# Kernel tuning notes

Measured on AMD Instinct MI355X. Metric: run time of the kernel, lower is better.

## Reference

```python
import jax, jax.numpy as jnp
import numpy as np

N, E, IN, HID, HEADS, ED, OUT = 50000, 600000, 128, 64, 4, 16, 2
NEG_SLOPE = 0.2  # PyG GATv2Conv default negative_slope


def glorot(key, shape):
    fan_in, fan_out = shape[0], shape[-1]
    s = jnp.sqrt(6.0 / (fan_in + fan_out))
    return jax.random.uniform(key, shape, jnp.float32, -s, s)


def setup_inputs() -> dict:
    key = jax.random.key(0)
    ks = jax.random.split(key, 16)
    return {
        "x": jax.random.normal(ks[0], (N, IN), jnp.float32),
        "edge_index": jax.random.randint(ks[1], (2, E), 0, N, jnp.int32),
        "edge_attr": jax.random.normal(ks[2], (E, ED), jnp.float32),
        # conv1: GATv2Conv(IN -> HID, heads=HEADS, concat=True, edge_dim=ED)
        "W1l": glorot(ks[3], (IN, HEADS * HID)), "b1l": jnp.zeros((HEADS * HID,), jnp.float32),
        "W1r": glorot(ks[4], (IN, HEADS * HID)), "b1r": jnp.zeros((HEADS * HID,), jnp.float32),
        "W1e": glorot(ks[5], (ED, HEADS * HID)), "b1e": jnp.zeros((HEADS * HID,), jnp.float32),
        "att1": glorot(ks[6], (HEADS, HID)),
        "bias1": jnp.zeros((HEADS * HID,), jnp.float32),
        # conv2: GATv2Conv(HEADS*HID -> HID, heads=1, concat=False, edge_dim=ED)
        "W2l": glorot(ks[7], (HEADS * HID, HID)), "b2l": jnp.zeros((HID,), jnp.float32),
        "W2r": glorot(ks[8], (HEADS * HID, HID)), "b2r": jnp.zeros((HID,), jnp.float32),
        "W2e": glorot(ks[9], (ED, HID)), "b2e": jnp.zeros((HID,), jnp.float32),
        "att2": glorot(ks[10], (1, HID)),
        "bias2": jnp.zeros((HID,), jnp.float32),
        # edge MLP: Linear(2*HID+ED -> HID) -> ReLU -> Linear(HID -> OUT)
        "Wm1": glorot(ks[11], (2 * HID + ED, HID)), "bm1": jnp.zeros((HID,), jnp.float32),
        "Wm2": glorot(ks[12], (HID, OUT)), "bm2": jnp.zeros((OUT,), jnp.float32),
    }


def gatv2_layer(x, src, dst, edge_attr, Wl, bl, Wr, br, We, be, att, bias, heads, ch, concat):
    n = x.shape[0]
    xl = (x @ Wl + bl).reshape(n, heads, ch)          # lin_l(source)
    xr = (x @ Wr + br).reshape(n, heads, ch)          # lin_r(target)
    xe = (edge_attr @ We + be).reshape(-1, heads, ch)  # lin_edge(edge_attr)
    m = jax.nn.leaky_relu(xl[src] + xr[dst] + xe, NEG_SLOPE)   # [E, H, C]
    logits = jnp.einsum('ehc,hc->eh', m, att)                  # [E, H]
    # segment softmax over incoming edges of each target node
    amax = jax.lax.stop_gradient(jax.ops.segment_max(logits, dst, num_segments=n))
    ex = jnp.exp(logits - amax[dst])
    denom = jax.ops.segment_sum(ex, dst, num_segments=n)
    alpha = ex / denom[dst]                                    # [E, H]
    out = jax.ops.segment_sum(xl[src] * alpha[..., None], dst, num_segments=n)  # [N, H, C]
    out = out.reshape(n, heads * ch) if concat else out.mean(axis=1)
    return out + bias


def reference(x, edge_index, edge_attr, W1l, b1l, W1r, b1r, W1e, b1e, att1, bias1,
              W2l, b2l, W2r, b2r, W2e, b2e, att2, bias2, Wm1, bm1, Wm2, bm2):
    src, dst = edge_index[0], edge_index[1]
    h = jax.nn.relu(gatv2_layer(x, src, dst, edge_attr, W1l, b1l, W1r, b1r, W1e, b1e, att1, bias1, HEADS, HID, True))
    h = jax.nn.relu(gatv2_layer(h, src, dst, edge_attr, W2l, b2l, W2r, b2r, W2e, b2e, att2, bias2, 1, HID, False))
    ef = jnp.concatenate([h[src], h[dst], edge_attr], axis=1)  # [E, 2*HID+ED]
    return jax.nn.relu(ef @ Wm1 + bm1) @ Wm2 + bm2             # [E, OUT]
```

## Files before the change

kernel.cpp:

```cpp
#include <hip/hip_runtime.h>
#include <math.h>

#define NN 50000
#define EE 600000
#define IND 128
#define HIDD 64
#define NH 4
#define EDD 16
#define OUTD 2
#define C1 256

typedef _Float16 h2 __attribute__((ext_vector_type(2)));

__device__ __forceinline__ float lrelu(float v){ return v > 0.f ? v : 0.2f*v; }
__device__ __forceinline__ unsigned short f2bf(float f){
    unsigned b = __float_as_uint(f);
    b += 0x7FFF + ((b >> 16) & 1);
    return (unsigned short)(b >> 16);
}
__device__ __forceinline__ float bf2f(unsigned short h){
    return __uint_as_float(((unsigned)h) << 16);
}

#if defined(__has_builtin)
#if __has_builtin(__builtin_amdgcn_fdot2)
#define HAS_FDOT2 1
#endif
#endif
__device__ __forceinline__ float fdot2(h2 a, h2 b, float c){
#ifdef HAS_FDOT2
    return __builtin_amdgcn_fdot2(a, b, c, false);
#else
    return fmaf((float)a[1], (float)b[1], fmaf((float)a[0], (float)b[0], c));
#endif
}

__global__ __launch_bounds__(256) void k_hist(const int* __restrict__ dst, int* __restrict__ cnt)
{
    int stride = gridDim.x * blockDim.x;
    for (int e = blockIdx.x * blockDim.x + threadIdx.x; e < EE; e += stride)
        atomicAdd(&cnt[dst[e]], 1);
}

__global__ __launch_bounds__(1024) void k_scan(const int* __restrict__ cnt, int* __restrict__ rs)
{
    __shared__ int wsum[16];
    __shared__ int wpref[16];
    int t = threadIdx.x, lane = t & 63, w = t >> 6;
    int running = 0;
    for (int base = 0; base < NN; base += 1024) {
        int idx = base + t;
        int v = (idx < NN) ? cnt[idx] : 0;
        int sc = v;
#pragma unroll
        for (int off = 1; off < 64; off <<= 1) {
            int u = __shfl_up(sc, off, 64);
            if (lane >= off) sc += u;
        }
        if (lane == 63) wsum[w] = sc;
        __syncthreads();
        if (w == 0 && lane < 16) {
            int x = wsum[lane];
#pragma unroll
            for (int off = 1; off < 16; off <<= 1) {
                int u = __shfl_up(x, off, 64);
                if (lane >= off) x += u;
            }
            wpref[lane] = x;
        }
        __syncthreads();
        int woff = (w == 0) ? 0 : wpref[w - 1];
        if (idx < NN) rs[idx] = running + woff + sc - v;
        running += wpref[15];
        __syncthreads();
    }
    if (t == 0) rs[NN] = running;
}

__global__ __launch_bounds__(256) void k_scatter(
    const int* __restrict__ src, const int* __restrict__ dst,
    const float* __restrict__ ea,
    const int* __restrict__ rs, int* __restrict__ cur,
    int* __restrict__ esrc, _Float16* __restrict__ ea_s, _Float16* __restrict__ ea_h)
{
    int stride = gridDim.x * blockDim.x;
    for (int e = blockIdx.x * blockDim.x + threadIdx.x; e < EE; e += stride) {
        int d = dst[e];
        int p = rs[d] + atomicAdd(&cur[d], 1);
        esrc[p] = src[e];
        const float4* s4 = (const float4*)(ea + (size_t)e * EDD);
        float4 a0 = s4[0], a1 = s4[1], a2 = s4[2], a3 = s4[3];
        union { h2 h[8]; uint4 u[2]; } pk;
        pk.h[0][0] = (_Float16)a0.x; pk.h[0][1] = (_Float16)a0.y;
        pk.h[1][0] = (_Float16)a0.z; pk.h[1][1] = (_Float16)a0.w;
        pk.h[2][0] = (_Float16)a1.x; pk.h[2][1] = (_Float16)a1.y;
        pk.h[3][0] = (_Float16)a1.z; pk.h[3][1] = (_Float16)a1.w;
        pk.h[4][0] = (_Float16)a2.x; pk.h[4][1] = (_Float16)a2.y;
        pk.h[5][0] = (_Float16)a2.z; pk.h[5][1] = (_Float16)a2.w;
        pk.h[6][0] = (_Float16)a3.x; pk.h[6][1] = (_Float16)a3.y;
        pk.h[7][0] = (_Float16)a3.z; pk.h[7][1] = (_Float16)a3.w;
        uint4* dq = (uint4*)(ea_s + (size_t)p * EDD);
        dq[0] = pk.u[0]; dq[1] = pk.u[1];
        uint4* hq = (uint4*)(ea_h + (size_t)e * EDD);
        hq[0] = pk.u[0]; hq[1] = pk.u[1];
    }
}

__global__ __launch_bounds__(256) void k_lin1(
    const float* __restrict__ x, const float* __restrict__ Wl, const float* __restrict__ bl,
    const float* __restrict__ Wr, const float* __restrict__ br,
    unsigned short* __restrict__ xl, float* __restrict__ xr)
{
    __shared__ float As[16 * IND];
    int t = threadIdx.x;
    int row0 = blockIdx.x * 16;
#pragma unroll
    for (int j = 0; j < 8; ++j) {
        int idx = t + j * 256;
        int r = idx >> 7, c = idx & 127;
        As[idx] = (row0 + r < NN) ? x[(size_t)(row0 + r) * IND + c] : 0.f;
    }
    __syncthreads();
    float accl[16], accr[16];
    float bL = bl[t], bR = br[t];
#pragma unroll
    for (int i = 0; i < 16; ++i) { accl[i] = bL; accr[i] = bR; }
    for (int k = 0; k < IND; k += 4) {
        float wl0 = Wl[(k+0) * C1 + t], wl1 = Wl[(k+1) * C1 + t];
        float wl2 = Wl[(k+2) * C1 + t], wl3 = Wl[(k+3) * C1 + t];
        float wr0 = Wr[(k+0) * C1 + t], wr1 = Wr[(k+1) * C1 + t];
        float wr2 = Wr[(k+2) * C1 + t], wr3 = Wr[(k+3) * C1 + t];
#pragma unroll
        for (int i = 0; i < 16; ++i) {
            float4 a = *((const float4*)&As[i * IND + k]);
            accl[i] = fmaf(a.x, wl0, accl[i]); accl[i] = fmaf(a.y, wl1, accl[i]);
            accl[i] = fmaf(a.z, wl2, accl[i]); accl[i] = fmaf(a.w, wl3, accl[i]);
            accr[i] = fmaf(a.x, wr0, accr[i]); accr[i] = fmaf(a.y, wr1, accr[i]);
            accr[i] = fmaf(a.z, wr2, accr[i]); accr[i] = fmaf(a.w, wr3, accr[i]);
        }
    }
#pragma unroll
    for (int i = 0; i < 16; ++i) {
        int r = row0 + i;
        if (r < NN) {
            xl[(size_t)r * C1 + t] = f2bf(accl[i]);
            xr[(size_t)r * C1 + t] = accr[i];
        }
    }
}

#define GAT1_EDGE(XU, U0, U1) {                                                \
    float4 xl4 = make_float4(bf2f((XU).x), bf2f((XU).y), bf2f((XU).z), bf2f((XU).w)); \
    union { uint4 u[2]; h2 h[8]; } eu_; eu_.u[0] = (U0); eu_.u[1] = (U1);      \
    float xex = sb4.x, xey = sb4.y, xez = sb4.z, xew = sb4.w;                  \
    _Pragma("unroll")                                                          \
    for (int kk = 0; kk < 8; ++kk) {                                           \
        h2 ev2 = eu_.h[kk];                                                    \
        xex = fdot2(ev2, Wh[0][kk], xex);                                      \
        xey = fdot2(ev2, Wh[1][kk], xey);                                      \
        xez = fdot2(ev2, Wh[2][kk], xez);                                      \
        xew = fdot2(ev2, Wh[3][kk], xew);                                      \
    }                                                                          \
    float vx = lrelu(xl4.x + xr4.x + xex);                                     \
    float vy = lrelu(xl4.y + xr4.y + xey);                                     \
    float vz = lrelu(xl4.z + xr4.z + xez);                                     \
    float vw = lrelu(xl4.w + xr4.w + xew);                                     \
    float p = vx * sa4.x + vy * sa4.y + vz * sa4.z + vw * sa4.w;               \
    p += __shfl_xor(p, 1, 64);                                                 \
    p += __shfl_xor(p, 2, 64);                                                 \
    p += __shfl_xor(p, 4, 64);                                                 \
    p += __shfl_xor(p, 8, 64);                                                 \
    float mn = fmaxf(m, p);                                                    \
    float scl = __expf(m - mn);                                                \
    float el  = __expf(p - mn);                                                \
    den = fmaf(den, scl, el);                                                  \
    acc.x = fmaf(acc.x, scl, el * xl4.x);                                      \
    acc.y = fmaf(acc.y, scl, el * xl4.y);                                      \
    acc.z = fmaf(acc.z, scl, el * xl4.z);                                      \
    acc.w = fmaf(acc.w, scl, el * xl4.w);                                      \
    m = mn;                                                                    \
}

__global__ __launch_bounds__(256, 3) void k_gat1(
    const int* __restrict__ rs, const int* __restrict__ esrc,
    const _Float16* __restrict__ ea_s, const float* __restrict__ We, const float* __restrict__ be,
    const float* __restrict__ att, const unsigned short* __restrict__ xl,
    const float* __restrict__ xr, float* __restrict__ h1)
{
    int t = threadIdx.x, lane = t & 63, w = t >> 6;
    int c4 = lane * 4;
    h2 Wh[4][8];
#pragma unroll
    for (int k = 0; k < 16; ++k) {
        float4 wv = *((const float4*)(We + k * C1 + c4));
        Wh[0][k>>1][k&1] = (_Float16)wv.x;
        Wh[1][k>>1][k&1] = (_Float16)wv.y;
        Wh[2][k>>1][k&1] = (_Float16)wv.z;
        Wh[3][k>>1][k&1] = (_Float16)wv.w;
    }
    float4 sb4 = *((const float4*)(be + c4));
    float4 sa4 = *((const float4*)(att + c4));
    for (int n = blockIdx.x * 4 + w; n < NN; n += gridDim.x * 4) {
        int beg = __builtin_amdgcn_readfirstlane(rs[n]);
        int end = __builtin_amdgcn_readfirstlane(rs[n + 1]);
        float4 xr4 = *((const float4*)(xr + (size_t)n * C1 + c4));
        float m = -INFINITY, den = 0.f;
        float4 acc = make_float4(0.f, 0.f, 0.f, 0.f);
        int i = beg;
        for (; i + 2 <= end; i += 2) {
            int s0 = esrc[i], s1 = esrc[i + 1];
            ushort4 xu0 = *((const ushort4*)(xl + (size_t)s0 * C1 + c4));
            ushort4 xu1 = *((const ushort4*)(xl + (size_t)s1 * C1 + c4));
            const uint4* ep = (const uint4*)(ea_s + (size_t)i * EDD);
            uint4 u00 = ep[0], u01 = ep[1];
            uint4 u10 = ep[2], u11 = ep[3];
            GAT1_EDGE(xu0, u00, u01);
            GAT1_EDGE(xu1, u10, u11);
        }
        if (i < end) {
            int s0 = esrc[i];
            ushort4 xu0 = *((const ushort4*)(xl + (size_t)s0 * C1 + c4));
            const uint4* ep = (const uint4*)(ea_s + (size_t)i * EDD);
            uint4 u00 = ep[0], u01 = ep[1];
            GAT1_EDGE(xu0, u00, u01);
        }
        float r = den > 0.f ? 1.f / den : 0.f;
        float4 o = make_float4(acc.x * r, acc.y * r, acc.z * r, acc.w * r);
        *((float4*)(h1 + (size_t)n * C1 + c4)) = o;
    }
}

__global__ __launch_bounds__(256) void k_lin2(
    const float* __restrict__ h1acc, const float* __restrict__ bias1,
    const float* __restrict__ Wl, const float* __restrict__ bl,
    const float* __restrict__ Wr, const float* __restrict__ br,
    unsigned short* __restrict__ xl2, float* __restrict__ xr2)
{
    __shared__ float As[16 * 260];
    int t = threadIdx.x;
    int row0 = blockIdx.x * 16;
    float b1 = bias1[t];
#pragma unroll
    for (int j = 0; j < 16; ++j) {
        float v = (row0 + j < NN) ? h1acc[(size_t)(row0 + j) * C1 + t] : 0.f;
        v = v + b1;
        As[j * 260 + t] = v > 0.f ? v : 0.f;
    }
    __syncthreads();
    int col = t & 63, g = t >> 6;
    float accl[4], accr[4];
    float bL = bl[col], bR = br[col];
#pragma unroll
    for (int i = 0; i < 4; ++i) { accl[i] = bL; accr[i] = bR; }
    for (int k = 0; k < C1; k += 4) {
        float wl0 = Wl[(k+0) * HIDD + col], wl1 = Wl[(k+1) * HIDD + col];
        float wl2 = Wl[(k+2) * HIDD + col], wl3 = Wl[(k+3) * HIDD + col];
        float wr0 = Wr[(k+0) * HIDD + col], wr1 = Wr[(k+1) * HIDD + col];
        float wr2 = Wr[(k+2) * HIDD + col], wr3 = Wr[(k+3) * HIDD + col];
#pragma unroll
        for (int i = 0; i < 4; ++i) {
            float4 a = *((const float4*)&As[(g * 4 + i) * 260 + k]);
            accl[i] = fmaf(a.x, wl0, accl[i]); accl[i] = fmaf(a.y, wl1, accl[i]);
            accl[i] = fmaf(a.z, wl2, accl[i]); accl[i] = fmaf(a.w, wl3, accl[i]);
            accr[i] = fmaf(a.x, wr0, accr[i]); accr[i] = fmaf(a.y, wr1, accr[i]);
            accr[i] = fmaf(a.z, wr2, accr[i]); accr[i] = fmaf(a.w, wr3, accr[i]);
        }
    }
#pragma unroll
    for (int i = 0; i < 4; ++i) {
        int r = row0 + g * 4 + i;
        if (r < NN) {
            xl2[(size_t)r * HIDD + col] = f2bf(accl[i]);
            xr2[(size_t)r * HIDD + col] = accr[i];
        }
    }
}

#define GAT2_EDGE(XU, U0, U1) {                                                \
    float xlv = bf2f(XU);                                                      \
    union { uint4 u[2]; h2 h[8]; } eu_; eu_.u[0] = (U0); eu_.u[1] = (U1);      \
    float xe = bev;                                                            \
    _Pragma("unroll")                                                          \
    for (int kk = 0; kk < 8; ++kk) xe = fdot2(eu_.h[kk], Wh2[kk], xe);         \
    float v = lrelu(xlv + xrv + xe);                                           \
    float p = v * sav;                                                         \
    p += __shfl_xor(p, 1, 64);                                                 \
    p += __shfl_xor(p, 2, 64);                                                 \
    p += __shfl_xor(p, 4, 64);                                                 \
    p += __shfl_xor(p, 8, 64);                                                 \
    p += __shfl_xor(p, 16, 64);                                                \
    p += __shfl_xor(p, 32, 64);                                                \
    float mn = fmaxf(m, p);                                                    \
    float scl = __expf(m - mn);                                                \
    float el  = __expf(p - mn);                                                \
    den = fmaf(den, scl, el);                                                  \
    acc = fmaf(acc, scl, el * xlv);                                            \
    m = mn;                                                                    \
}

__global__ __launch_bounds__(256) void k_gat2(
    const int* __restrict__ rs, const int* __restrict__ esrc,
    const _Float16* __restrict__ ea_s, const float* __restrict__ We, const float* __restrict__ be,
    const float* __restrict__ att, const unsigned short* __restrict__ xl,
    const float* __restrict__ xr, const float* __restrict__ bias2, float* __restrict__ h2v)
{
    int t = threadIdx.x, lane = t & 63, w = t >> 6;
    h2 Wh2[8];
#pragma unroll
    for (int k = 0; k < 16; ++k) Wh2[k>>1][k&1] = (_Float16)We[k * HIDD + lane];
    float bev = be[lane], sav = att[lane], b2 = bias2[lane];
    for (int n = blockIdx.x * 4 + w; n < NN; n += gridDim.x * 4) {
        int beg = __builtin_amdgcn_readfirstlane(rs[n]);
        int end = __builtin_amdgcn_readfirstlane(rs[n + 1]);
        float xrv = xr[(size_t)n * HIDD + lane];
        float m = -INFINITY, den = 0.f, acc = 0.f;
        int i = beg;
        for (; i + 2 <= end; i += 2) {
            int s0 = esrc[i], s1 = esrc[i + 1];
            unsigned short xu0 = xl[(size_t)s0 * HIDD + lane];
            unsigned short xu1 = xl[(size_t)s1 * HIDD + lane];
            const uint4* ep = (const uint4*)(ea_s + (size_t)i * EDD);
            uint4 u00 = ep[0], u01 = ep[1];
            uint4 u10 = ep[2], u11 = ep[3];
            GAT2_EDGE(xu0, u00, u01);
            GAT2_EDGE(xu1, u10, u11);
        }
        if (i < end) {
            int s0 = esrc[i];
            unsigned short xu0 = xl[(size_t)s0 * HIDD + lane];
            const uint4* ep = (const uint4*)(ea_s + (size_t)i * EDD);
            uint4 u00 = ep[0], u01 = ep[1];
            GAT2_EDGE(xu0, u00, u01);
        }
        float r = den > 0.f ? 1.f / den : 0.f;
        float o = fmaf(acc, r, b2);
        h2v[(size_t)n * HIDD + lane] = o > 0.f ? o : 0.f;
    }
}

__global__ __launch_bounds__(256) void k_pq(
    const float* __restrict__ h2, const float* __restrict__ Wm1,
    unsigned short* __restrict__ P, unsigned short* __restrict__ Q)
{
    __shared__ float As[16 * 68];
    int t = threadIdx.x;
    int row0 = blockIdx.x * 16;
    {
        int r = t >> 4, cc = (t & 15) * 4;
        float4 v = *((const float4*)(h2 + (size_t)(row0 + r) * HIDD + cc));
        *((float4*)&As[r * 68 + cc]) = v;
    }
    __syncthreads();
    int col = t & 63, g = t >> 6;
    float accP[4] = {0.f, 0.f, 0.f, 0.f}, accQ[4] = {0.f, 0.f, 0.f, 0.f};
    for (int k = 0; k < 64; k += 4) {
        float wp0 = Wm1[(k+0) * HIDD + col], wp1 = Wm1[(k+1) * HIDD + col];
        float wp2 = Wm1[(k+2) * HIDD + col], wp3 = Wm1[(k+3) * HIDD + col];
        float wq0 = Wm1[(64+k+0) * HIDD + col], wq1 = Wm1[(64+k+1) * HIDD + col];
        float wq2 = Wm1[(64+k+2) * HIDD + col], wq3 = Wm1[(64+k+3) * HIDD + col];
#pragma unroll
        for (int i = 0; i < 4; ++i) {
            float4 a = *((const float4*)&As[(g * 4 + i) * 68 + k]);
            accP[i] = fmaf(a.x, wp0, accP[i]); accP[i] = fmaf(a.y, wp1, accP[i]);
            accP[i] = fmaf(a.z, wp2, accP[i]); accP[i] = fmaf(a.w, wp3, accP[i]);
            accQ[i] = fmaf(a.x, wq0, accQ[i]); accQ[i] = fmaf(a.y, wq1, accQ[i]);
            accQ[i] = fmaf(a.z, wq2, accQ[i]); accQ[i] = fmaf(a.w, wq3, accQ[i]);
        }
    }
#pragma unroll
    for (int i = 0; i < 4; ++i) {
        int r = row0 + g * 4 + i;
        P[(size_t)r * HIDD + col] = f2bf(accP[i]);
        Q[(size_t)r * HIDD + col] = f2bf(accQ[i]);
    }
}

__global__ __launch_bounds__(256, 3) void k_edge(
    const int* __restrict__ src, const int* __restrict__ dst,
    const unsigned short* __restrict__ P, const unsigned short* __restrict__ Q,
    const _Float16* __restrict__ ea_h,
    const float* __restrict__ Wm1, const float* __restrict__ bm1,
    const float* __restrict__ Wm2, const float* __restrict__ bm2,
    float* __restrict__ out)
{
    int t = threadIdx.x, lane = t & 63, w = t >> 6;
    int sub = lane & 15, grp = lane >> 4;
    int c4 = sub * 4;
    h2 Wh[4][8];
#pragma unroll
    for (int k = 0; k < 16; ++k) {
        float4 wv = *((const float4*)(Wm1 + (size_t)(128 + k) * HIDD + c4));
        Wh[0][k>>1][k&1] = (_Float16)wv.x;
        Wh[1][k>>1][k&1] = (_Float16)wv.y;
        Wh[2][k>>1][k&1] = (_Float16)wv.z;
        Wh[3][k>>1][k&1] = (_Float16)wv.w;
    }
    float4 b1 = *((const float4*)(bm1 + c4));
    float w200 = Wm2[(c4+0)*2], w201 = Wm2[(c4+0)*2+1];
    float w210 = Wm2[(c4+1)*2], w211 = Wm2[(c4+1)*2+1];
    float w220 = Wm2[(c4+2)*2], w221 = Wm2[(c4+2)*2+1];
    float w230 = Wm2[(c4+3)*2], w231 = Wm2[(c4+3)*2+1];
    float b20 = bm2[0], b21 = bm2[1];
    for (int base = blockIdx.x * 16 + w * 4; base < EE; base += gridDim.x * 16) {
        int e = base + grp;
        int s = src[e], d = dst[e];
        ushort4 pu = *((const ushort4*)(P + (size_t)s * HIDD + c4));
        ushort4 qu = *((const ushort4*)(Q + (size_t)d * HIDD + c4));
        union { uint4 u[2]; h2 h[8]; } eu_;
        const uint4* ep = (const uint4*)(ea_h + (size_t)e * EDD);
        eu_.u[0] = ep[0]; eu_.u[1] = ep[1];
        float4 hsum = b1;
#pragma unroll
        for (int kk = 0; kk < 8; ++kk) {
            h2 ev2 = eu_.h[kk];
            hsum.x = fdot2(ev2, Wh[0][kk], hsum.x);
            hsum.y = fdot2(ev2, Wh[1][kk], hsum.y);
            hsum.z = fdot2(ev2, Wh[2][kk], hsum.z);
            hsum.w = fdot2(ev2, Wh[3][kk], hsum.w);
        }
        float hx = fmaxf(hsum.x + bf2f(pu.x) + bf2f(qu.x), 0.f);
        float hy = fmaxf(hsum.y + bf2f(pu.y) + bf2f(qu.y), 0.f);
        float hz = fmaxf(hsum.z + bf2f(pu.z) + bf2f(qu.z), 0.f);
        float hw = fmaxf(hsum.w + bf2f(pu.w) + bf2f(qu.w), 0.f);
        float p0 = hx * w200 + hy * w210 + hz * w220 + hw * w230;
        float p1 = hx * w201 + hy * w211 + hz * w221 + hw * w231;
        p0 += __shfl_xor(p0, 1, 64);
        p0 += __shfl_xor(p0, 2, 64);
        p0 += __shfl_xor(p0, 4, 64);
        p0 += __shfl_xor(p0, 8, 64);
        p1 += __shfl_xor(p1, 1, 64);
        p1 += __shfl_xor(p1, 2, 64);
        p1 += __shfl_xor(p1, 4, 64);
        p1 += __shfl_xor(p1, 8, 64);
        if (sub == 0) ((float2*)out)[e] = make_float2(p0 + b20, p1 + b21);
    }
}

extern "C" void kernel_launch(void* const* d_in, const int* in_sizes, int n_in,
                              void* d_out, int out_size, void* d_ws, size_t ws_size,
                              hipStream_t stream)
{
    const float* x    = (const float*)d_in[0];
    const int*   ei   = (const int*)d_in[1];
    const float* ea   = (const float*)d_in[2];
    const float* W1l  = (const float*)d_in[3];
    const float* b1l  = (const float*)d_in[4];
    const float* W1r  = (const float*)d_in[5];
    const float* b1r  = (const float*)d_in[6];
    const float* W1e  = (const float*)d_in[7];
    const float* b1e  = (const float*)d_in[8];
    const float* att1 = (const float*)d_in[9];
    const float* bias1= (const float*)d_in[10];
    const float* W2l  = (const float*)d_in[11];
    const float* b2l  = (const float*)d_in[12];
    const float* W2r  = (const float*)d_in[13];
    const float* b2r  = (const float*)d_in[14];
    const float* W2e  = (const float*)d_in[15];
    const float* b2e  = (const float*)d_in[16];
    const float* att2 = (const float*)d_in[17];
    const float* bias2= (const float*)d_in[18];
    const float* Wm1  = (const float*)d_in[19];
    const float* bm1  = (const float*)d_in[20];
    const float* Wm2  = (const float*)d_in[21];
    const float* bm2  = (const float*)d_in[22];
    float* out = (float*)d_out;
    const int* srcp = ei;
    const int* dstp = ei + EE;

    float* ws = (float*)d_ws;
    const size_t NC1  = (size_t)NN * C1;
    const size_t NH64 = (size_t)NN * HIDD;
    const size_t EAH  = (size_t)EE * EDD / 2;
    size_t o_xl1u = 0;
    size_t o_xr1  = o_xl1u + NC1 / 2;
    size_t o_xl2u = 0;
    size_t o_xr2  = o_xl2u + NH64 / 2;
    size_t o_h2   = o_xr2 + NH64;
    size_t o_Pu   = o_h2 + NH64;
    size_t o_Qu   = o_Pu + NH64 / 2;
    size_t o_h1   = o_xr1 + NC1;
    size_t o_ea_s = o_h1 + NC1;
    size_t o_ea_h = o_ea_s + EAH;
    size_t o_cnt  = o_ea_h + EAH;
    size_t o_rs   = o_cnt + 2 * (size_t)NN;
    size_t o_esrc = o_rs + (size_t)NN + 8;

    unsigned short* xl1u = (unsigned short*)(ws + o_xl1u);
    unsigned short* xl2u = (unsigned short*)(ws + o_xl2u);
    unsigned short* Pu   = (unsigned short*)(ws + o_Pu);
    unsigned short* Qu   = (unsigned short*)(ws + o_Qu);
    _Float16* ea_s = (_Float16*)(ws + o_ea_s);
    _Float16* ea_h = (_Float16*)(ws + o_ea_h);
    int* cnt  = (int*)(ws + o_cnt);
    int* cur  = cnt + NN;
    int* rs   = (int*)(ws + o_rs);
    int* esrc = (int*)(ws + o_esrc);

    hipMemsetAsync(cnt, 0, 2 * (size_t)NN * sizeof(int), stream);

    dim3 blk(256);
    k_hist<<<1024, blk, 0, stream>>>(dstp, cnt);
    k_scan<<<1, 1024, 0, stream>>>(cnt, rs);
    k_scatter<<<1024, blk, 0, stream>>>(srcp, dstp, ea, rs, cur, esrc, ea_s, ea_h);

    k_lin1<<<3125, blk, 0, stream>>>(x, W1l, b1l, W1r, b1r, xl1u, ws + o_xr1);
    k_gat1<<<2048, blk, 0, stream>>>(rs, esrc, ea_s, W1e, b1e, att1,
                                     xl1u, ws + o_xr1, ws + o_h1);
    k_lin2<<<3125, blk, 0, stream>>>(ws + o_h1, bias1, W2l, b2l, W2r, b2r,
                                     xl2u, ws + o_xr2);
    k_gat2<<<2048, blk, 0, stream>>>(rs, esrc, ea_s, W2e, b2e, att2,
                                     xl2u, ws + o_xr2, bias2, ws + o_h2);
    k_pq<<<3125, blk, 0, stream>>>(ws + o_h2, Wm1, Pu, Qu);
    k_edge<<<2048, blk, 0, stream>>>(srcp, dstp, Pu, Qu, ea_h,
                                     Wm1, bm1, Wm2, bm2, out);
}
```

Before: 663.4 us.

## Use fp16 dot2 in node linear kernels and batch four edges per softmax update

The two node-linear kernels now store their input tile in shared memory as packed fp16, convert the weights to fp16 pairs, and accumulate with fdot2. Each block also handles 32 rows instead of 16, which halves the grid and reuses each weight load across more rows. Both GAT aggregation loops now compute four edge logits before doing one online-softmax rescale, which cuts exp and rescale work and exposes more independent gathers. The cost is lower input precision in the linear layers, more registers per thread, and lower occupancy in lin1.

```diff
diff --git a/kernel.cpp b/kernel.cpp
--- a/kernel.cpp
+++ b/kernel.cpp
@@ -20,6 +20,9 @@
 }
 __device__ __forceinline__ float bf2f(unsigned short h){
     return __uint_as_float(((unsigned)h) << 16);
+}
+__device__ __forceinline__ h2 f2h2(float a, float b){
+    h2 r; r[0] = (_Float16)a; r[1] = (_Float16)b; return r;
 }
 
 #if defined(__has_builtin)
@@ -91,14 +94,10 @@
         const float4* s4 = (const float4*)(ea + (size_t)e * EDD);
         float4 a0 = s4[0], a1 = s4[1], a2 = s4[2], a3 = s4[3];
         union { h2 h[8]; uint4 u[2]; } pk;
-        pk.h[0][0] = (_Float16)a0.x; pk.h[0][1] = (_Float16)a0.y;
-        pk.h[1][0] = (_Float16)a0.z; pk.h[1][1] = (_Float16)a0.w;
-        pk.h[2][0] = (_Float16)a1.x; pk.h[2][1] = (_Float16)a1.y;
-        pk.h[3][0] = (_Float16)a1.z; pk.h[3][1] = (_Float16)a1.w;
-        pk.h[4][0] = (_Float16)a2.x; pk.h[4][1] = (_Float16)a2.y;
-        pk.h[5][0] = (_Float16)a2.z; pk.h[5][1] = (_Float16)a2.w;
-        pk.h[6][0] = (_Float16)a3.x; pk.h[6][1] = (_Float16)a3.y;
-        pk.h[7][0] = (_Float16)a3.z; pk.h[7][1] = (_Float16)a3.w;
+        pk.h[0] = f2h2(a0.x, a0.y); pk.h[1] = f2h2(a0.z, a0.w);
+        pk.h[2] = f2h2(a1.x, a1.y); pk.h[3] = f2h2(a1.z, a1.w);
+        pk.h[4] = f2h2(a2.x, a2.y); pk.h[5] = f2h2(a2.z, a2.w);
+        pk.h[6] = f2h2(a3.x, a3.y); pk.h[7] = f2h2(a3.z, a3.w);
         uint4* dq = (uint4*)(ea_s + (size_t)p * EDD);
         dq[0] = pk.u[0]; dq[1] = pk.u[1];
         uint4* hq = (uint4*)(ea_h + (size_t)e * EDD);
@@ -111,36 +110,41 @@
     const float* __restrict__ Wr, const float* __restrict__ br,
     unsigned short* __restrict__ xl, float* __restrict__ xr)
 {
-    __shared__ float As[16 * IND];
+    __shared__ h2 As[32 * 64];
     int t = threadIdx.x;
-    int row0 = blockIdx.x * 16;
-#pragma unroll
-    for (int j = 0; j < 8; ++j) {
+    int row0 = blockIdx.x * 32;
+#pragma unroll
+    for (int j = 0; j < 4; ++j) {
         int idx = t + j * 256;
-        int r = idx >> 7, c = idx & 127;
-        As[idx] = (row0 + r < NN) ? x[(size_t)(row0 + r) * IND + c] : 0.f;
+        int r = idx >> 5, c4 = (idx & 31) * 4;
+        float4 v = (row0 + r < NN) ? *((const float4*)(x + (size_t)(row0 + r) * IND + c4))
+                                   : make_float4(0.f, 0.f, 0.f, 0.f);
+        union { h2 h[2]; uint2 u; } pk;
+        pk.h[0] = f2h2(v.x, v.y); pk.h[1] = f2h2(v.z, v.w);
+        *((uint2*)&As[r * 64 + (c4 >> 1)]) = pk.u;
     }
     __syncthreads();
-    float accl[16], accr[16];
+    float accl[32], accr[32];
     float bL = bl[t], bR = br[t];
 #pragma unroll
-    for (int i = 0; i < 16; ++i) { accl[i] = bL; accr[i] = bR; }
+    for (int i = 0; i < 32; ++i) { accl[i] = bL; accr[i] = bR; }
     for (int k = 0; k < IND; k += 4) {
-        float wl0 = Wl[(k+0) * C1 + t], wl1 = Wl[(k+1) * C1 + t];
-        float wl2 = Wl[(k+2) * C1 + t], wl3 = Wl[(k+3) * C1 + t];
-        float wr0 = Wr[(k+0) * C1 + t], wr1 = Wr[(k+1) * C1 + t];
-        float wr2 = Wr[(k+2) * C1 + t], wr3 = Wr[(k+3) * C1 + t];
-#pragma unroll
-        for (int i = 0; i < 16; ++i) {
-            float4 a = *((const float4*)&As[i * IND + k]);
-            accl[i] = fmaf(a.x, wl0, accl[i]); accl[i] = fmaf(a.y, wl1, accl[i]);
-            accl[i] = fmaf(a.z, wl2, accl[i]); accl[i] = fmaf(a.w, wl3, accl[i]);
-            accr[i] = fmaf(a.x, wr0, accr[i]); accr[i] = fmaf(a.y, wr1, accr[i]);
-            accr[i] = fmaf(a.z, wr2, accr[i]); accr[i] = fmaf(a.w, wr3, accr[i]);
-        }
-    }
-#pragma unroll
-    for (int i = 0; i < 16; ++i) {
+        h2 wl01 = f2h2(Wl[(k+0) * C1 + t], Wl[(k+1) * C1 + t]);
+        h2 wl23 = f2h2(Wl[(k+2) * C1 + t], Wl[(k+3) * C1 + t]);
+        h2 wr01 = f2h2(Wr[(k+0) * C1 + t], Wr[(k+1) * C1 + t]);
+        h2 wr23 = f2h2(Wr[(k+2) * C1 + t], Wr[(k+3) * C1 + t]);
+#pragma unroll
+        for (int i = 0; i < 32; ++i) {
+            union { uint2 u; h2 h[2]; } av;
+            av.u = *((const uint2*)&As[i * 64 + (k >> 1)]);
+            accl[i] = fdot2(av.h[0], wl01, accl[i]);
+            accl[i] = fdot2(av.h[1], wl23, accl[i]);
+            accr[i] = fdot2(av.h[0], wr01, accr[i]);
+            accr[i] = fdot2(av.h[1], wr23, accr[i]);
+        }
+    }
+#pragma unroll
+    for (int i = 0; i < 32; ++i) {
         int r = row0 + i;
         if (r < NN) {
             xl[(size_t)r * C1 + t] = f2bf(accl[i]);
@@ -149,8 +153,8 @@
     }
 }
 
-#define GAT1_EDGE(XU, U0, U1) {                                                \
-    float4 xl4 = make_float4(bf2f((XU).x), bf2f((XU).y), bf2f((XU).z), bf2f((XU).w)); \
+#define GAT1_P(XU, U0, U1, PP, XL4) {                                          \
+    XL4 = make_float4(bf2f((XU).x), bf2f((XU).y), bf2f((XU).z), bf2f((XU).w)); \
     union { uint4 u[2]; h2 h[8]; } eu_; eu_.u[0] = (U0); eu_.u[1] = (U1);      \
     float xex = sb4.x, xey = sb4.y, xez = sb4.z, xew = sb4.w;                  \
     _Pragma("unroll")                                                          \
@@ -161,15 +165,20 @@
         xez = fdot2(ev2, Wh[2][kk], xez);                                      \
         xew = fdot2(ev2, Wh[3][kk], xew);                                      \
     }                                                                          \
-    float vx = lrelu(xl4.x + xr4.x + xex);                                     \
-    float vy = lrelu(xl4.y + xr4.y + xey);                                     \
-    float vz = lrelu(xl4.z + xr4.z + xez);                                     \
-    float vw = lrelu(xl4.w + xr4.w + xew);                                     \
-    float p = vx * sa4.x + vy * sa4.y + vz * sa4.z + vw * sa4.w;               \
-    p += __shfl_xor(p, 1, 64);                                                 \
-    p += __shfl_xor(p, 2, 64);                                                 \
-    p += __shfl_xor(p, 4, 64);                                                 \
-    p += __shfl_xor(p, 8, 64);                                                 \
+    float vx = lrelu(XL4.x + xr4.x + xex);                                     \
+    float vy = lrelu(XL4.y + xr4.y + xey);                                     \
+    float vz = lrelu(XL4.z + xr4.z + xez);                                     \
+    float vw = lrelu(XL4.w + xr4.w + xew);                                     \
+    PP = vx * sa4.x + vy * sa4.y + vz * sa4.z + vw * sa4.w;                    \
+    PP += __shfl_xor(PP, 1, 64);                                               \
+    PP += __shfl_xor(PP, 2, 64);                                               \
+    PP += __shfl_xor(PP, 4, 64);                                               \
+    PP += __shfl_xor(PP, 8, 64);                                               \
+}
+
+#define GAT1_EDGE(XU, U0, U1) {                                                \
+    float4 xl4; float p;                                                       \
+    GAT1_P(XU, U0, U1, p, xl4);                                                \
     float mn = fmaxf(m, p);                                                    \
     float scl = __expf(m - mn);                                                \
     float el  = __expf(p - mn);                                                \
@@ -207,17 +216,34 @@
         float m = -INFINITY, den = 0.f;
         float4 acc = make_float4(0.f, 0.f, 0.f, 0.f);
         int i = beg;
-        for (; i + 2 <= end; i += 2) {
-            int s0 = esrc[i], s1 = esrc[i + 1];
+        for (; i + 4 <= end; i += 4) {
+            int s0 = esrc[i], s1 = esrc[i + 1], s2 = esrc[i + 2], s3 = esrc[i + 3];
             ushort4 xu0 = *((const ushort4*)(xl + (size_t)s0 * C1 + c4));
             ushort4 xu1 = *((const ushort4*)(xl + (size_t)s1 * C1 + c4));
+            ushort4 xu2 = *((const ushort4*)(xl + (size_t)s2 * C1 + c4));
+            ushort4 xu3 = *((const ushort4*)(xl + (size_t)s3 * C1 + c4));
             const uint4* ep = (const uint4*)(ea_s + (size_t)i * EDD);
-            uint4 u00 = ep[0], u01 = ep[1];
-            uint4 u10 = ep[2], u11 = ep[3];
-            GAT1_EDGE(xu0, u00, u01);
-            GAT1_EDGE(xu1, u10, u11);
-        }
-        if (i < end) {
+            uint4 u0 = ep[0], u1 = ep[1], u2 = ep[2], u3 = ep[3];
+            uint4 u4 = ep[4], u5 = ep[5], u6 = ep[6], u7 = ep[7];
+            float p0, p1, p2, p3;
+            float4 xa, xb, xc, xd;
+            GAT1_P(xu0, u0, u1, p0, xa);
+            GAT1_P(xu1, u2, u3, p1, xb);
+            GAT1_P(xu2, u4, u5, p2, xc);
+            GAT1_P(xu3, u6, u7, p3, xd);
+            float pm = fmaxf(fmaxf(p0, p1), fmaxf(p2, p3));
+            float mn = fmaxf(m, pm);
+            float scl = __expf(m - mn);
+            float e0 = __expf(p0 - mn), e1 = __expf(p1 - mn);
+            float e2 = __expf(p2 - mn), e3 = __expf(p3 - mn);
+            den = fmaf(den, scl, (e0 + e1) + (e2 + e3));
+            acc.x = fmaf(acc.x, scl, fmaf(e0, xa.x, fmaf(e1, xb.x, fmaf(e2, xc.x, e3 * xd.x))));
+            acc.y = fmaf(acc.y, scl, fmaf(e0, xa.y, fmaf(e1, xb.y, fmaf(e2, xc.y, e3 * xd.y))));
+            acc.z = fmaf(acc.z, scl, fmaf(e0, xa.z, fmaf(e1, xb.z, fmaf(e2, xc.z, e3 * xd.z))));
+            acc.w = fmaf(acc.w, scl, fmaf(e0, xa.w, fmaf(e1, xb.w, fmaf(e2, xc.w, e3 * xd.w))));
+            m = mn;
+        }
+        for (; i < end; ++i) {
             int s0 = esrc[i];
             ushort4 xu0 = *((const ushort4*)(xl + (size_t)s0 * C1 + c4));
             const uint4* ep = (const uint4*)(ea_s + (size_t)i * EDD);
@@ -236,39 +262,41 @@
     const float* __restrict__ Wr, const float* __restrict__ br,
     unsigned short* __restrict__ xl2, float* __restrict__ xr2)
 {
-    __shared__ float As[16 * 260];
+    __shared__ h2 As[32 * 130];
     int t = threadIdx.x;
-    int row0 = blockIdx.x * 16;
-    float b1 = bias1[t];
-#pragma unroll
-    for (int j = 0; j < 16; ++j) {
+    int row0 = blockIdx.x * 32;
+    float b1v = bias1[t];
+#pragma unroll
+    for (int j = 0; j < 32; ++j) {
         float v = (row0 + j < NN) ? h1acc[(size_t)(row0 + j) * C1 + t] : 0.f;
-        v = v + b1;
-        As[j * 260 + t] = v > 0.f ? v : 0.f;
+        v = v + b1v;
+        v = v > 0.f ? v : 0.f;
+        As[j * 130 + (t >> 1)][t & 1] = (_Float16)v;
     }
     __syncthreads();
     int col = t & 63, g = t >> 6;
-    float accl[4], accr[4];
+    float accl[8], accr[8];
     float bL = bl[col], bR = br[col];
 #pragma unroll
-    for (int i = 0; i < 4; ++i) { accl[i] = bL; accr[i] = bR; }
+    for (int i = 0; i < 8; ++i) { accl[i] = bL; accr[i] = bR; }
     for (int k = 0; k < C1; k += 4) {
-        float wl0 = Wl[(k+0) * HIDD + col], wl1 = Wl[(k+1) * HIDD + col];
-        float wl2 = Wl[(k+2) * HIDD + col], wl3 = Wl[(k+3) * HIDD + col];
-        float wr0 = Wr[(k+0) * HIDD + col], wr1 = Wr[(k+1) * HIDD + col];
-        float wr2 = Wr[(k+2) * HIDD + col], wr3 = Wr[(k+3) * HIDD + col];
-#pragma unroll
-        for (int i = 0; i < 4; ++i) {
-            float4 a = *((const float4*)&As[(g * 4 + i) * 260 + k]);
-            accl[i] = fmaf(a.x, wl0, accl[i]); accl[i] = fmaf(a.y, wl1, accl[i]);
-            accl[i] = fmaf(a.z, wl2, accl[i]); accl[i] = fmaf(a.w, wl3, accl[i]);
-            accr[i] = fmaf(a.x, wr0, accr[i]); accr[i] = fmaf(a.y, wr1, accr[i]);
-            accr[i] = fmaf(a.z, wr2, accr[i]); accr[i] = fmaf(a.w, wr3, accr[i]);
-        }
-    }
-#pragma unroll
-    for (int i = 0; i < 4; ++i) {
-        int r = row0 + g * 4 + i;
+        h2 wl01 = f2h2(Wl[(k+0) * HIDD + col], Wl[(k+1) * HIDD + col]);
+        h2 wl23 = f2h2(Wl[(k+2) * HIDD + col], Wl[(k+3) * HIDD + col]);
+        h2 wr01 = f2h2(Wr[(k+0) * HIDD + col], Wr[(k+1) * HIDD + col]);
+        h2 wr23 = f2h2(Wr[(k+2) * HIDD + col], Wr[(k+3) * HIDD + col]);
+#pragma unroll
+        for (int i = 0; i < 8; ++i) {
+            union { uint2 u; h2 h[2]; } av;
+            av.u = *((const uint2*)&As[(g * 8 + i) * 130 + (k >> 1)]);
+            accl[i] = fdot2(av.h[0], wl01, accl[i]);
+            accl[i] = fdot2(av.h[1], wl23, accl[i]);
+            accr[i] = fdot2(av.h[0], wr01, accr[i]);
+            accr[i] = fdot2(av.h[1], wr23, accr[i]);
+        }
+    }
+#pragma unroll
+    for (int i = 0; i < 8; ++i) {
+        int r = row0 + g * 8 + i;
         if (r < NN) {
             xl2[(size_t)r * HIDD + col] = f2bf(accl[i]);
             xr2[(size_t)r * HIDD + col] = accr[i];
@@ -276,20 +304,25 @@
     }
 }
 
-#define GAT2_EDGE(XU, U0, U1) {                                                \
-    float xlv = bf2f(XU);                                                      \
+#define GAT2_P(XU, U0, U1, PP, XLV) {                                          \
+    XLV = bf2f(XU);                                                            \
     union { uint4 u[2]; h2 h[8]; } eu_; eu_.u[0] = (U0); eu_.u[1] = (U1);      \
     float xe = bev;                                                            \
     _Pragma("unroll")                                                          \
     for (int kk = 0; kk < 8; ++kk) xe = fdot2(eu_.h[kk], Wh2[kk], xe);         \
-    float v = lrelu(xlv + xrv + xe);                                           \
-    float p = v * sav;                                                         \
-    p += __shfl_xor(p, 1, 64);                                                 \
-    p += __shfl_xor(p, 2, 64);                                                 \
-    p += __shfl_xor(p, 4, 64);                                                 \
-    p += __shfl_xor(p, 8, 64);                                                 \
-    p += __shfl_xor(p, 16, 64);                                                \
-    p += __shfl_xor(p, 32, 64);                                                \
+    float v = lrelu(XLV + xrv + xe);                                           \
+    PP = v * sav;                                                              \
+    PP += __shfl_xor(PP, 1, 64);                                               \
+    PP += __shfl_xor(PP, 2, 64);                                               \
+    PP += __shfl_xor(PP, 4, 64);                                               \
+    PP += __shfl_xor(PP, 8, 64);                                               \
+    PP += __shfl_xor(PP, 16, 64);                                              \
+    PP += __shfl_xor(PP, 32, 64);                                              \
+}
+
+#define GAT2_EDGE(XU, U0, U1) {                                                \
+    float xlv; float p;                                                        \
+    GAT2_P(XU, U0, U1, p, xlv);                                                \
     float mn = fmaxf(m, p);                                                    \
     float scl = __expf(m - mn);                                                \
     float el  = __expf(p - mn);                                                \
@@ -315,17 +348,31 @@
         float xrv = xr[(size_t)n * HIDD + lane];
         float m = -INFINITY, den = 0.f, acc = 0.f;
         int i = beg;
-        for (; i + 2 <= end; i += 2) {
-            int s0 = esrc[i], s1 = esrc[i + 1];
+        for (; i + 4 <= end; i += 4) {
+            int s0 = esrc[i], s1 = esrc[i + 1], s2 = esrc[i + 2], s3 = esrc[i + 3];
             unsigned short xu0 = xl[(size_t)s0 * HIDD + lane];
             unsigned short xu1 = xl[(size_t)s1 * HIDD + lane];
+            unsigned short xu2 = xl[(size_t)s2 * HIDD + lane];
+            unsigned short xu3 = xl[(size_t)s3 * HIDD + lane];
             const uint4* ep = (const uint4*)(ea_s + (size_t)i * EDD);
-            uint4 u00 = ep[0], u01 = ep[1];
-            uint4 u10 = ep[2], u11 = ep[3];
-            GAT2_EDGE(xu0, u00, u01);
-            GAT2_EDGE(xu1, u10, u11);
-        }
-        if (i < end) {
+            uint4 u0 = ep[0], u1 = ep[1], u2 = ep[2], u3 = ep[3];
+            uint4 u4 = ep[4], u5 = ep[5], u6 = ep[6], u7 = ep[7];
+            float p0, p1, p2, p3;
+            float xa, xb, xc, xd;
+            GAT2_P(xu0, u0, u1, p0, xa);
+            GAT2_P(xu1, u2, u3, p1, xb);
+            GAT2_P(xu2, u4, u5, p2, xc);
+            GAT2_P(xu3, u6, u7, p3, xd);
+            float pm = fmaxf(fmaxf(p0, p1), fmaxf(p2, p3));
+            float mn = fmaxf(m, pm);
+            float scl = __expf(m - mn);
+            float e0 = __expf(p0 - mn), e1 = __expf(p1 - mn);
+            float e2 = __expf(p2 - mn), e3 = __expf(p3 - mn);
+            den = fmaf(den, scl, (e0 + e1) + (e2 + e3));
+            acc = fmaf(acc, scl, fmaf(e0, xa, fmaf(e1, xb, fmaf(e2, xc, e3 * xd))));
+            m = mn;
+        }
+        for (; i < end; ++i) {
             int s0 = esrc[i];
             unsigned short xu0 = xl[(size_t)s0 * HIDD + lane];
             const uint4* ep = (const uint4*)(ea_s + (size_t)i * EDD);
@@ -503,10 +550,10 @@
     k_scan<<<1, 1024, 0, stream>>>(cnt, rs);
     k_scatter<<<1024, blk, 0, stream>>>(srcp, dstp, ea, rs, cur, esrc, ea_s, ea_h);
 
-    k_lin1<<<3125, blk, 0, stream>>>(x, W1l, b1l, W1r, b1r, xl1u, ws + o_xr1);
+    k_lin1<<<1563, blk, 0, stream>>>(x, W1l, b1l, W1r, b1r, xl1u, ws + o_xr1);
     k_gat1<<<2048, blk, 0, stream>>>(rs, esrc, ea_s, W1e, b1e, att1,
                                      xl1u, ws + o_xr1, ws + o_h1);
-    k_lin2<<<3125, blk, 0, stream>>>(ws + o_h1, bias1, W2l, b2l, W2r, b2r,
+    k_lin2<<<1563, blk, 0, stream>>>(ws + o_h1, bias1, W2l, b2l, W2r, b2r,
                                      xl2u, ws + o_xr2);
     k_gat2<<<2048, blk, 0, stream>>>(rs, esrc, ea_s, W2e, b2e, att2,
                                      xl2u, ws + o_xr2, bias2, ws + o_h2);
```

New measurement: 610.6 us. 1.09x faster.
